# Optimization experiments

Hardware: AMD Instinct MI355X
Metric: run time of the kernel (lower is better)

The kernel has to match this reference:

```python
import jax, jax.numpy as jnp
import numpy as np
from jax import lax

TEMP = 0.01          # relay smoothing temperature (init kwarg temp=0.01)
MESH_SCALE = 0.01    # grid spacing on the unit Preisach triangle
T_STEPS = 4096       # length of applied-field history


def _triangle_mesh(scale):
    # grid points (beta, alpha) on the unit triangle with beta <= alpha,
    # mirroring create_triangle_mesh(mesh_scale)
    n = int(round(1.0 / scale)) + 1  # 101 points per side
    g = np.linspace(0.0, 1.0, n)
    b, a = np.meshgrid(g, g, indexing='ij')
    keep = b <= a
    pts = np.stack([b[keep], a[keep]], axis=-1)  # [N, 2], N = n*(n+1)/2 = 5151
    return pts.astype(np.float32)


def setup_inputs() -> dict:
    key = jax.random.key(0)
    k_h, k_d = jax.random.split(key)
    mesh_points = jnp.asarray(_triangle_mesh(MESH_SCALE))          # [N, 2]
    h = jax.random.uniform(k_h, (T_STEPS,), dtype=jnp.float32)     # normalized fields in [0,1]
    raw_density = jax.random.normal(k_d, (mesh_points.shape[0],), dtype=jnp.float32)
    raw_offset = jnp.zeros((1,), jnp.float32)
    raw_scale = jnp.zeros((1,), jnp.float32)
    raw_slope = jnp.zeros((1,), jnp.float32)
    return {
        'h': h,
        'mesh_points': mesh_points,
        'raw_density': raw_density,
        'raw_offset': raw_offset,
        'raw_scale': raw_scale,
        'raw_slope': raw_slope,
    }


def _get_states(h, mesh_points, temp):
    # Temperature-smoothed Preisach relay recurrence over the mesh.
    # state starts at negative saturation (-1); field starts at 0.
    beta = mesh_points[:, 0]   # switch-down thresholds
    alpha = mesh_points[:, 1]  # switch-up thresholds
    n = mesh_points.shape[0]

    def step(carry, ht):
        s, f = carry
        # increasing field: relays with alpha <= h flip toward +1 (smoothed)
        up = s + (1.0 - s) * jax.nn.sigmoid((ht - alpha) / temp)
        # decreasing field: relays with beta >= h flip toward -1 (smoothed)
        dn = s + (-1.0 - s) * jax.nn.sigmoid((beta - ht) / temp)
        s_new = jnp.where(ht > f, up, dn)
        return (s_new, ht), s_new

    init = (-jnp.ones((n,), h.dtype), jnp.zeros((), h.dtype))
    _, states = lax.scan(step, init, h)  # [T, N]
    return states


def reference(h, mesh_points, raw_density, raw_offset, raw_scale, raw_slope):
    states = _get_states(h, mesh_points, TEMP)  # [T, N]
    # gpytorch Interval(lower, upper) transform: lower + (upper-lower)*sigmoid(raw)
    density = jax.nn.sigmoid(raw_density)                    # Interval(0, 1)
    offset = -10.0 + 20.0 * jax.nn.sigmoid(raw_offset)       # Interval(-10, 10)
    scale = 20.0 * jax.nn.sigmoid(raw_scale)                 # Interval(0, 20)
    slope = -20.0 + 40.0 * jax.nn.sigmoid(raw_slope)         # Interval(-20, 20)
    # weighted magnetization: sum_n density_n * s_tn / sum_n density_n
    m = (states @ density) / jnp.sum(density)                # [T]
    return scale * m + h * slope + offset                    # [T]
```

## Files before the change

kernel.cpp:

```cpp
#include <hip/hip_runtime.h>
#include <hip/hip_bf16.h>
#include <stdint.h>

#define TSTEPS   4096
#define C_CHUNKS 128
#define L_STEPS  32
#define JPAD     128

__device__ __forceinline__ float fast_exp2(float x){ return __builtin_amdgcn_exp2f(x); }
__device__ __forceinline__ float fast_rcp (float x){ return __builtin_amdgcn_rcpf(x); }
__device__ __forceinline__ float sigmoid_f(float x){
  return fast_rcp(1.0f + fast_exp2(-1.4426950408889634f * x));
}

__global__ __launch_bounds__(256) void k0_prep(
    const float* __restrict__ h, const float* __restrict__ raw_density,
    const float* __restrict__ raw_offset, const float* __restrict__ raw_scale,
    const float* __restrict__ raw_slope,
    int N, float* __restrict__ tab, uint32_t* __restrict__ umask,
    float* __restrict__ Dws, float* __restrict__ out)
{
  const int tid = threadIdx.x;
  const int c   = blockIdx.x;
  const int t0  = c * L_STEPS;
  const float C = 144.26950408889634f;

  if (tid < 64) {
    const int  l    = tid;
    const int  t    = t0 + l;
    bool bit = false;
    if (l < L_STEPS) {
      const float ht = h[t];
      const float hp = (t > 0) ? h[t - 1] : 0.0f;
      bit = ht > hp;
    }
    const uint64_t m = __ballot(bit);
    if (l == 0) umask[c] = (uint32_t)(m & 0xffffffffull);
  }

  #pragma unroll
  for (int pass = 0; pass < 16; ++pass) {
    const int item = pass * 256 + tid;
    const int trel = item >> 7;
    const int j    = item & 127;
    if (j <= 100) {
      const int   t  = t0 + trel;
      const float ht = h[t];
      const float hp = (t > 0) ? h[t - 1] : 0.0f;
      const bool  up = ht > hp;
      const float x  = (float)j * 0.01f;
      const float arg = up ? (x - ht) * C : (ht - x) * C;
      const float g   = fast_rcp(1.0f + fast_exp2(arg));
      tab[(size_t)t * JPAD + j] = up ? g : -g;
    }
  }

  if (c == 0) {
    __shared__ float red[256];
    float loc = 0.f;
    for (int j = tid; j < N; j += 256) loc += sigmoid_f(raw_density[j]);
    red[tid] = loc;
    __syncthreads();
    for (int st = 128; st > 0; st >>= 1) {
      if (tid < st) red[tid] += red[tid + st];
      __syncthreads();
    }
    if (tid == 0) Dws[0] = red[0];
    const float offset = -10.0f + 20.0f * sigmoid_f(raw_offset[0]);
    const float slope  = -20.0f + 40.0f * sigmoid_f(raw_slope[0]);
    for (int t = tid; t < TSTEPS; t += 256) out[t] = fmaf(h[t], slope, offset);
  }
}

__global__ __launch_bounds__(256) void k1_affine(
    const float* __restrict__ tab, const uint32_t* __restrict__ umask,
    const float* __restrict__ mesh,
    int N, int Np, float* __restrict__ Aw, float* __restrict__ Bw)
{
  const int tid = threadIdx.x;
  const int i   = blockIdx.x * 256 + tid;
  const int c   = blockIdx.y;

  float beta = 0.f, alpha = 0.f;
  if (i < N) { beta = mesh[2*i]; alpha = mesh[2*i+1]; }
  const int ia = (int)(alpha * 100.0f + 0.5f);
  const int ib = (int)(beta  * 100.0f + 0.5f);

  const uint32_t um   = umask[c];
  const float*   tabc = tab + (size_t)c * L_STEPS * JPAD;

  float A = 1.0f, B = 0.0f;
  #pragma unroll
  for (int tl = 0; tl < L_STEPS; ++tl) {
    const int   idx = ((um >> tl) & 1u) ? ia : ib;
    const float v   = tabc[tl * JPAD + idx];
    const float a   = 1.0f - fabsf(v);
    A = A * a;
    B = fmaf(a, B, v);
  }
  Aw[(size_t)c * Np + i] = A;
  Bw[(size_t)c * Np + i] = B;
}

__global__ __launch_bounds__(256) void k2_scan(
    const float* __restrict__ Aw, const float* __restrict__ Bw,
    float* __restrict__ Sw, int Np)
{
  const int i = blockIdx.x * 256 + threadIdx.x;
  float s = -1.0f;
  #pragma unroll 8
  for (int c = 0; c < C_CHUNKS; ++c) {
    const size_t off = (size_t)c * Np + i;
    Sw[off] = s;
    s = fmaf(Aw[off], s, Bw[off]);
  }
}

__global__ __launch_bounds__(256) void k3_states(
    const float* __restrict__ tab, const uint32_t* __restrict__ umask,
    const float* __restrict__ mesh, const float* __restrict__ raw_density,
    const float* __restrict__ Sw, const float* __restrict__ Dws,
    const float* __restrict__ raw_scale,
    int N, int Np, float* __restrict__ out)
{
  const int tid  = threadIdx.x;
  const int i    = blockIdx.x * 256 + tid;
  const int c    = blockIdx.y;
  const int lane = tid & 63;
  const int t0   = c * L_STEPS;

  float beta = 0.f, alpha = 0.f, d = 0.f;
  if (i < N) { beta = mesh[2*i]; alpha = mesh[2*i+1]; d = sigmoid_f(raw_density[i]); }
  const int ia = (int)(alpha * 100.0f + 0.5f);
  const int ib = (int)(beta  * 100.0f + 0.5f);

  const uint32_t um   = umask[c];
  const float*   tabc = tab + (size_t)c * L_STEPS * JPAD;

  float s = Sw[(size_t)c * Np + i];
  float cur[L_STEPS];
  #pragma unroll
  for (int tl = 0; tl < L_STEPS; ++tl) {
    const int   idx = ((um >> tl) & 1u) ? ia : ib;
    const float v   = tabc[tl * JPAD + idx];
    const float a   = 1.0f - fabsf(v);
    s = fmaf(a, s, v);
    cur[tl] = d * s;
  }

  #pragma unroll
  for (int k = 0; k < 5; ++k) {
    const bool bb = (lane >> k) & 1;
    #pragma unroll
    for (int j = 0; j < (L_STEPS >> (k + 1)); ++j) {
      const float x = bb ? cur[2*j + 1] : cur[2*j];
      const float y = bb ? cur[2*j]     : cur[2*j + 1];
      cur[j] = x + __shfl_xor(y, 1 << k, 64);
    }
  }
  const float val = cur[0] + __shfl_xor(cur[0], 32, 64);

  const float scale = 20.0f * sigmoid_f(raw_scale[0]);
  const float coef  = scale / Dws[0];
  if (lane < L_STEPS) atomicAdd(&out[t0 + lane], coef * val);
}

extern "C" void kernel_launch(void* const* d_in, const int* in_sizes, int n_in,
                              void* d_out, int out_size, void* d_ws, size_t ws_size,
                              hipStream_t stream)
{
  const float* h           = (const float*)d_in[0];
  const float* mesh        = (const float*)d_in[1];
  const float* raw_density = (const float*)d_in[2];
  const float* raw_offset  = (const float*)d_in[3];
  const float* raw_scale   = (const float*)d_in[4];
  const float* raw_slope   = (const float*)d_in[5];
  float* out = (float*)d_out;

  const int N  = in_sizes[2];
  const int P  = (N + 255) / 256;
  const int Np = P * 256;

  float* ws   = (float*)d_ws;
  float* tab  = ws;
  float* Aw   = tab + (size_t)TSTEPS * JPAD;
  float* Bw   = Aw  + (size_t)C_CHUNKS * Np;
  float* Sw   = Bw  + (size_t)C_CHUNKS * Np;
  float* Dws  = Sw  + (size_t)C_CHUNKS * Np;
  uint32_t* umask = (uint32_t*)(Dws + 1);

  dim3 gridPC(P, C_CHUNKS);
  k0_prep  <<<C_CHUNKS, 256, 0, stream>>>(h, raw_density, raw_offset, raw_scale,
                                          raw_slope, N, tab, umask, Dws, out);
  k1_affine<<<gridPC,  256, 0, stream>>>(tab, umask, mesh, N, Np, Aw, Bw);
  k2_scan  <<<P,       256, 0, stream>>>(Aw, Bw, Sw, Np);
  k3_states<<<gridPC,  256, 0, stream>>>(tab, umask, mesh, raw_density, Sw, Dws,
                                         raw_scale, N, Np, out);
}
```

Before: 42.50 us.

## Fuse sigmoid table construction into affine and state kernels via shared memory

Removes the separate prep kernel and its global lookup table. Each block of the affine and state kernels recomputes its chunk's 32x101 sigmoid table and up/down mask into LDS, then gathers from shared memory. This saves one kernel launch and the global table write/read, at the cost of redundant exp/rcp work in every block plus a block barrier. The density reduction and affine output init move into the first block of the affine kernel.

Measured after the change: 43.17 us. About the same (+1.6%).

```diff
diff --git a/kernel.cpp b/kernel.cpp
--- a/kernel.cpp
+++ b/kernel.cpp
@@ -5,7 +5,7 @@
 #define TSTEPS   4096
 #define C_CHUNKS 128
 #define L_STEPS  32
-#define JPAD     128
+#define JROW     104
 
 __device__ __forceinline__ float fast_exp2(float x){ return __builtin_amdgcn_exp2f(x); }
 __device__ __forceinline__ float fast_rcp (float x){ return __builtin_amdgcn_rcpf(x); }
@@ -13,30 +13,20 @@
   return fast_rcp(1.0f + fast_exp2(-1.4426950408889634f * x));
 }
 
-__global__ __launch_bounds__(256) void k0_prep(
-    const float* __restrict__ h, const float* __restrict__ raw_density,
-    const float* __restrict__ raw_offset, const float* __restrict__ raw_scale,
-    const float* __restrict__ raw_slope,
-    int N, float* __restrict__ tab, uint32_t* __restrict__ umask,
-    float* __restrict__ Dws, float* __restrict__ out)
+__device__ __forceinline__ uint32_t build_table(
+    const float* __restrict__ h, int t0, float (*tabs)[JROW], int tid)
 {
-  const int tid = threadIdx.x;
-  const int c   = blockIdx.x;
-  const int t0  = c * L_STEPS;
   const float C = 144.26950408889634f;
 
-  if (tid < 64) {
-    const int  l    = tid;
-    const int  t    = t0 + l;
-    bool bit = false;
-    if (l < L_STEPS) {
-      const float ht = h[t];
-      const float hp = (t > 0) ? h[t - 1] : 0.0f;
-      bit = ht > hp;
-    }
-    const uint64_t m = __ballot(bit);
-    if (l == 0) umask[c] = (uint32_t)(m & 0xffffffffull);
+  const int  lane = tid & 63;
+  bool bit = false;
+  if (lane < L_STEPS) {
+    const int t = t0 + lane;
+    const float ht = h[t];
+    const float hp = (t > 0) ? h[t - 1] : 0.0f;
+    bit = ht > hp;
   }
+  const uint32_t um = (uint32_t)(__ballot(bit) & 0xffffffffull);
 
   #pragma unroll
   for (int pass = 0; pass < 16; ++pass) {
@@ -51,11 +41,43 @@
       const float x  = (float)j * 0.01f;
       const float arg = up ? (x - ht) * C : (ht - x) * C;
       const float g   = fast_rcp(1.0f + fast_exp2(arg));
-      tab[(size_t)t * JPAD + j] = up ? g : -g;
+      tabs[trel][j] = up ? g : -g;
     }
   }
+  __syncthreads();
+  return um;
+}
 
-  if (c == 0) {
+__global__ __launch_bounds__(256) void kA_affine(
+    const float* __restrict__ h, const float* __restrict__ mesh,
+    const float* __restrict__ raw_density, const float* __restrict__ raw_offset,
+    const float* __restrict__ raw_slope,
+    int N, int Np, float* __restrict__ Aw, float* __restrict__ Bw,
+    float* __restrict__ Dws, float* __restrict__ out)
+{
+  __shared__ float tabs[L_STEPS][JROW];
+  const int tid = threadIdx.x;
+  const int i   = blockIdx.x * 256 + tid;
+  const int c   = blockIdx.y;
+  const uint32_t um = build_table(h, c * L_STEPS, tabs, tid);
+
+  float beta = 0.f, alpha = 0.f;
+  if (i < N) { beta = mesh[2*i]; alpha = mesh[2*i+1]; }
+  const int ia = (int)(alpha * 100.0f + 0.5f);
+  const int ib = (int)(beta  * 100.0f + 0.5f);
+
+  float A = 1.0f, B = 0.0f;
+  #pragma unroll
+  for (int tl = 0; tl < L_STEPS; ++tl) {
+    const float v = tabs[tl][((um >> tl) & 1u) ? ia : ib];
+    const float a = 1.0f - fabsf(v);
+    A = A * a;
+    B = fmaf(a, B, v);
+  }
+  Aw[(size_t)c * Np + i] = A;
+  Bw[(size_t)c * Np + i] = B;
+
+  if (blockIdx.x == 0 && c == 0) {
     __shared__ float red[256];
     float loc = 0.f;
     for (int j = tid; j < N; j += 256) loc += sigmoid_f(raw_density[j]);
@@ -72,36 +94,6 @@
   }
 }
 
-__global__ __launch_bounds__(256) void k1_affine(
-    const float* __restrict__ tab, const uint32_t* __restrict__ umask,
-    const float* __restrict__ mesh,
-    int N, int Np, float* __restrict__ Aw, float* __restrict__ Bw)
-{
-  const int tid = threadIdx.x;
-  const int i   = blockIdx.x * 256 + tid;
-  const int c   = blockIdx.y;
-
-  float beta = 0.f, alpha = 0.f;
-  if (i < N) { beta = mesh[2*i]; alpha = mesh[2*i+1]; }
-  const int ia = (int)(alpha * 100.0f + 0.5f);
-  const int ib = (int)(beta  * 100.0f + 0.5f);
-
-  const uint32_t um   = umask[c];
-  const float*   tabc = tab + (size_t)c * L_STEPS * JPAD;
-
-  float A = 1.0f, B = 0.0f;
-  #pragma unroll
-  for (int tl = 0; tl < L_STEPS; ++tl) {
-    const int   idx = ((um >> tl) & 1u) ? ia : ib;
-    const float v   = tabc[tl * JPAD + idx];
-    const float a   = 1.0f - fabsf(v);
-    A = A * a;
-    B = fmaf(a, B, v);
-  }
-  Aw[(size_t)c * Np + i] = A;
-  Bw[(size_t)c * Np + i] = B;
-}
-
 __global__ __launch_bounds__(256) void k2_scan(
     const float* __restrict__ Aw, const float* __restrict__ Bw,
     float* __restrict__ Sw, int Np)
@@ -116,34 +108,31 @@
   }
 }
 
-__global__ __launch_bounds__(256) void k3_states(
-    const float* __restrict__ tab, const uint32_t* __restrict__ umask,
-    const float* __restrict__ mesh, const float* __restrict__ raw_density,
-    const float* __restrict__ Sw, const float* __restrict__ Dws,
-    const float* __restrict__ raw_scale,
+__global__ __launch_bounds__(256) void kB_states(
+    const float* __restrict__ h, const float* __restrict__ mesh,
+    const float* __restrict__ raw_density, const float* __restrict__ Sw,
+    const float* __restrict__ Dws, const float* __restrict__ raw_scale,
     int N, int Np, float* __restrict__ out)
 {
+  __shared__ float tabs[L_STEPS][JROW];
   const int tid  = threadIdx.x;
   const int i    = blockIdx.x * 256 + tid;
   const int c    = blockIdx.y;
   const int lane = tid & 63;
   const int t0   = c * L_STEPS;
+  const uint32_t um = build_table(h, t0, tabs, tid);
 
   float beta = 0.f, alpha = 0.f, d = 0.f;
   if (i < N) { beta = mesh[2*i]; alpha = mesh[2*i+1]; d = sigmoid_f(raw_density[i]); }
   const int ia = (int)(alpha * 100.0f + 0.5f);
   const int ib = (int)(beta  * 100.0f + 0.5f);
 
-  const uint32_t um   = umask[c];
-  const float*   tabc = tab + (size_t)c * L_STEPS * JPAD;
-
   float s = Sw[(size_t)c * Np + i];
   float cur[L_STEPS];
   #pragma unroll
   for (int tl = 0; tl < L_STEPS; ++tl) {
-    const int   idx = ((um >> tl) & 1u) ? ia : ib;
-    const float v   = tabc[tl * JPAD + idx];
-    const float a   = 1.0f - fabsf(v);
+    const float v = tabs[tl][((um >> tl) & 1u) ? ia : ib];
+    const float a = 1.0f - fabsf(v);
     s = fmaf(a, s, v);
     cur[tl] = d * s;
   }
@@ -160,8 +149,7 @@
   }
   const float val = cur[0] + __shfl_xor(cur[0], 32, 64);
 
-  const float scale = 20.0f * sigmoid_f(raw_scale[0]);
-  const float coef  = scale / Dws[0];
+  const float coef = 20.0f * sigmoid_f(raw_scale[0]) / Dws[0];
   if (lane < L_STEPS) atomicAdd(&out[t0 + lane], coef * val);
 }
 
@@ -181,19 +169,16 @@
   const int P  = (N + 255) / 256;
   const int Np = P * 256;
 
-  float* ws   = (float*)d_ws;
-  float* tab  = ws;
-  float* Aw   = tab + (size_t)TSTEPS * JPAD;
-  float* Bw   = Aw  + (size_t)C_CHUNKS * Np;
-  float* Sw   = Bw  + (size_t)C_CHUNKS * Np;
-  float* Dws  = Sw  + (size_t)C_CHUNKS * Np;
-  uint32_t* umask = (uint32_t*)(Dws + 1);
+  float* ws  = (float*)d_ws;
+  float* Aw  = ws;
+  float* Bw  = Aw + (size_t)C_CHUNKS * Np;
+  float* Sw  = Bw + (size_t)C_CHUNKS * Np;
+  float* Dws = Sw + (size_t)C_CHUNKS * Np;
 
   dim3 gridPC(P, C_CHUNKS);
-  k0_prep  <<<C_CHUNKS, 256, 0, stream>>>(h, raw_density, raw_offset, raw_scale,
-                                          raw_slope, N, tab, umask, Dws, out);
-  k1_affine<<<gridPC,  256, 0, stream>>>(tab, umask, mesh, N, Np, Aw, Bw);
-  k2_scan  <<<P,       256, 0, stream>>>(Aw, Bw, Sw, Np);
-  k3_states<<<gridPC,  256, 0, stream>>>(tab, umask, mesh, raw_density, Sw, Dws,
-                                         raw_scale, N, Np, out);
+  kA_affine<<<gridPC, 256, 0, stream>>>(h, mesh, raw_density, raw_offset,
+                                        raw_slope, N, Np, Aw, Bw, Dws, out);
+  k2_scan  <<<P,      256, 0, stream>>>(Aw, Bw, Sw, Np);
+  kB_states<<<gridPC, 256, 0, stream>>>(h, mesh, raw_density, Sw, Dws,
+                                        raw_scale, N, Np, out);
 }
```
